# Kernel tuning notes

Measured on AMD Instinct MI355X. Metric: run time of the kernel, lower is better.

Reference implementation:

```python
import jax, jax.numpy as jnp
import numpy as np

H, D = 8, 8          # num_heads, hidden_size (head dim)
SCALE = 0.25         # Hopfield beta/scaling
STEPS = 3            # update_steps_max
LN_EPS = 1e-5


def ln(x, g, b):
    m = x.mean(-1, keepdims=True)
    v = ((x - m) ** 2).mean(-1, keepdims=True)
    return (x - m) * jax.lax.rsqrt(v + LN_EPS) * g + b


def setup_inputs() -> dict:
    key = jax.random.key(0)
    ks = jax.random.split(key, 8)
    B, N, E = 32, 512, 512
    P = H * D  # 64 virtual hopfield dim
    s = lambda k, shape: jax.random.normal(k, shape, jnp.float32) * 0.05
    return dict(
        x=jax.random.normal(ks[0], (B, N, E), jnp.float32),
        g_q=jnp.ones((E,), jnp.float32), b_q=jnp.zeros((E,), jnp.float32),
        g_k=jnp.ones((E,), jnp.float32), b_k=jnp.zeros((E,), jnp.float32),
        g_v=jnp.ones((E,), jnp.float32), b_v=jnp.zeros((E,), jnp.float32),
        Wq=s(ks[1], (P, E)), bq=jnp.zeros((P,), jnp.float32),
        Wk=s(ks[2], (P, E)), bk=jnp.zeros((P,), jnp.float32),
        Wv=s(ks[3], (P, E)), bv=jnp.zeros((P,), jnp.float32),
        Wo=s(ks[4], (E, P)), bo=jnp.zeros((E,), jnp.float32),
        Wl=s(ks[5], (1, N * E)), bl=jnp.zeros((1,), jnp.float32),
    )


def reference(x, g_q, b_q, g_k, b_k, g_v, b_v,
              Wq, bq, Wk, bk, Wv, bv, Wo, bo, Wl, bl):
    B, N, E = x.shape
    # LayerNorm on state (query), stored (key), projection (value) patterns
    q = (ln(x, g_q, b_q) @ Wq.T + bq).reshape(B, N, H, D)
    k = (ln(x, g_k, b_k) @ Wk.T + bk).reshape(B, N, H, D)
    v = (ln(x, g_v, b_v) @ Wv.T + bv).reshape(B, N, H, D)
    # iterative Hopfield retrieval: xi <- softmax(beta * xi K^T) K
    xi = q
    for _ in range(STEPS):
        a = jax.nn.softmax(SCALE * jnp.einsum('bihd,bjhd->bhij', xi, k), axis=-1)
        xi = jnp.einsum('bhij,bjhd->bihd', a, k)
    # final association with value patterns
    a = jax.nn.softmax(SCALE * jnp.einsum('bihd,bjhd->bhij', xi, k), axis=-1)
    o = jnp.einsum('bhij,bjhd->bihd', a, v).reshape(B, N, H * D)
    o = o @ Wo.T + bo              # (B, N, E) out projection
    y = o.reshape(B, N * E) @ Wl.T + bl  # (B, 1) classifier head
    return y.reshape(-1)           # flatten(start_dim=0) -> (B,)
```

## Files before the change

kernel.cpp:

```cpp
#include <hip/hip_runtime.h>

#define E_DIM 512
#define N_DIM 512
#define B_DIM 32
#define H_DIM 8
#define D_DIM 8
#define P3    192

typedef _Float16 half_t;
typedef __attribute__((ext_vector_type(2))) _Float16 half2v;
typedef __attribute__((ext_vector_type(4))) _Float16 half4v;
typedef __attribute__((ext_vector_type(8))) _Float16 half8v;
typedef __attribute__((ext_vector_type(4))) float f32x4;

#define PB_STRIDE 36
#define XS_STRIDE 520

__device__ inline float block_reduce_256(float v) {
    __shared__ float red[4];
    #pragma unroll
    for (int m = 32; m >= 1; m >>= 1) v += __shfl_xor(v, m);
    int w = threadIdx.x >> 6;
    if ((threadIdx.x & 63) == 0) red[w] = v;
    __syncthreads();
    if (threadIdx.x == 0) v = red[0] + red[1] + red[2] + red[3];
    return v;
}

__device__ inline half8v cvt8(float4 a, float4 b) {
    half8v h;
    h[0] = (half_t)a.x; h[1] = (half_t)a.y; h[2] = (half_t)a.z; h[3] = (half_t)a.w;
    h[4] = (half_t)b.x; h[5] = (half_t)b.y; h[6] = (half_t)b.z; h[7] = (half_t)b.w;
    return h;
}

__device__ inline half2v pk2(float a, float b) {
    return __builtin_bit_cast(half2v, __builtin_amdgcn_cvt_pkrtz(a, b));
}

__global__ __launch_bounds__(256) void prep_w(const float* __restrict__ Wq,
                        const float* __restrict__ Wk, const float* __restrict__ Wv,
                        const float* __restrict__ gq, const float* __restrict__ gk,
                        const float* __restrict__ gv,
                        const float* __restrict__ bnq, const float* __restrict__ bnk,
                        const float* __restrict__ bnv,
                        const float* __restrict__ bq, const float* __restrict__ bk,
                        const float* __restrict__ bv,
                        const float* __restrict__ bl,
                        half_t* __restrict__ WthF, float* __restrict__ colsum,
                        float* __restrict__ b2, float* __restrict__ y,
                        float* __restrict__ c0acc) {
    int pp = blockIdx.x;
    int which = pp >> 6, p = pp & 63;
    int ct = pp >> 4, c16 = pp & 15;
    const float* W  = (which == 0) ? Wq  : (which == 1) ? Wk  : Wv;
    const float* g  = (which == 0) ? gq  : (which == 1) ? gk  : gv;
    const float* bn = (which == 0) ? bnq : (which == 1) ? bnk : bnv;
    const float* bb = (which == 0) ? bq  : (which == 1) ? bk  : bv;
    int t = threadIdx.x;
    if (pp == 0) {
        if (t < 32) y[t] = bl[0];
        if (t == 32) c0acc[0] = 0.f;
    }
    float cs = 0.f, dt = 0.f;
    #pragma unroll
    for (int l = 0; l < 2; ++l) {
        int e = t + l * 256;
        float wv = W[p * E_DIM + e];
        half_t wh = (half_t)(wv * g[e]);
        int k32 = e >> 5, g2 = (e >> 3) & 3, j = e & 7;
        WthF[(((size_t)(ct * 16 + k32) * 64) + g2 * 16 + c16) * 8 + j] = wh;
        cs += (float)wh;
        dt += wv * bn[e];
    }
    cs = block_reduce_256(cs);
    __syncthreads();
    dt = block_reduce_256(dt);
    if (t == 0) { colsum[pp] = cs; b2[pp] = dt + bb[p]; }
}

__global__ __launch_bounds__(256) void ln_qkv_wl2(const float* __restrict__ x,
                                              const half_t* __restrict__ WthF,
                                              const float* __restrict__ b2,
                                              const float* __restrict__ colsum,
                                              half_t* __restrict__ qkv16,
                                              const float* __restrict__ Wl,
                                              const float* __restrict__ Wo,
                                              const float* __restrict__ bo,
                                              float* __restrict__ Wl2,
                                              float* __restrict__ c0acc) {
    __shared__ half_t Xs[16 * XS_STRIDE];
    __shared__ float stats[16][2];
    if (blockIdx.x < 1024) {
        const int t = threadIdx.x;
        const int lane = t & 63;
        const int w = t >> 6;
        const int g2 = lane >> 4, c16 = lane & 15;
        const int row0 = blockIdx.x * 16;
        {
            const int row = t >> 4, c = t & 15;
            const float4* xrow = (const float4*)(x + (size_t)(row0 + row) * E_DIM);
            float sx = 0.f, sxx = 0.f;
            #pragma unroll
            for (int l = 0; l < 8; ++l) {
                int f4 = c + l * 16;
                float4 a = xrow[f4];
                sx  += a.x + a.y + a.z + a.w;
                sxx += a.x*a.x + a.y*a.y + a.z*a.z + a.w*a.w;
                half4v h;
                h[0] = (half_t)a.x; h[1] = (half_t)a.y;
                h[2] = (half_t)a.z; h[3] = (half_t)a.w;
                *(half4v*)&Xs[row * XS_STRIDE + f4 * 4] = h;
            }
            #pragma unroll
            for (int m = 1; m <= 8; m <<= 1) {
                sx += __shfl_xor(sx, m); sxx += __shfl_xor(sxx, m);
            }
            if (c == 0) {
                float mean = sx * (1.f / E_DIM);
                float var  = sxx * (1.f / E_DIM) - mean * mean;
                stats[row][0] = mean;
                stats[row][1] = rsqrtf(var + 1e-5f);
            }
        }
        __syncthreads();
        f32x4 acc[3] = {{0.f,0.f,0.f,0.f},{0.f,0.f,0.f,0.f},{0.f,0.f,0.f,0.f}};
        const half_t* wf = WthF + (size_t)w * 3 * 16 * 512;
        #pragma unroll 4
        for (int k32 = 0; k32 < 16; ++k32) {
            half8v af = *(const half8v*)&Xs[c16 * XS_STRIDE + k32 * 32 + g2 * 8];
            #pragma unroll
            for (int nt = 0; nt < 3; ++nt) {
                half8v bf = *(const half8v*)(wf + ((size_t)(nt * 16 + k32)) * 512 + lane * 8);
                acc[nt] = __builtin_amdgcn_mfma_f32_16x16x32_f16(af, bf, acc[nt], 0, 0, 0);
            }
        }
        #pragma unroll
        for (int nt = 0; nt < 3; ++nt) {
            int pp = w * 48 + nt * 16 + c16;
            float cs = colsum[pp], bb = b2[pp];
            int which = pp >> 6, p = pp & 63;
            int h = p >> 3, d = p & 7;
            half_t* dst0 = qkv16 + (size_t)which * (B_DIM * H_DIM * N_DIM * D_DIM);
            #pragma unroll
            for (int r = 0; r < 4; ++r) {
                int rowi = g2 * 4 + r;
                float val = stats[rowi][1] * (acc[nt][r] - stats[rowi][0] * cs) + bb;
                int ng = row0 + rowi;
                int b = ng >> 9, n = ng & 511;
                dst0[(((size_t)(b * H_DIM + h)) * N_DIM + n) * D_DIM + d] = (half_t)val;
            }
        }
    } else {
        const int blk = blockIdx.x - 1024;
        const int t = threadIdx.x;
        const int lane = t & 63;
        const int w = t >> 6;
        const int g2 = lane >> 4, c16 = lane & 15;
        const int n0 = blk * 16;
        const int pcol = w * 16;
        f32x4 acc = {0.f, 0.f, 0.f, 0.f};
        float pc = 0.f;
        const float* arow = Wl + (size_t)(n0 + c16) * E_DIM;
        #pragma unroll 2
        for (int k0 = 0; k0 < E_DIM; k0 += 32) {
            int kbase = k0 + g2 * 8;
            float4 a0 = *(const float4*)(arow + kbase);
            float4 a1 = *(const float4*)(arow + kbase + 4);
            if (w == 0) {
                float4 b0 = *(const float4*)(bo + kbase);
                float4 b1 = *(const float4*)(bo + kbase + 4);
                pc += a0.x*b0.x + a0.y*b0.y + a0.z*b0.z + a0.w*b0.w
                    + a1.x*b1.x + a1.y*b1.y + a1.z*b1.z + a1.w*b1.w;
            }
            half8v af = cvt8(a0, a1);
            half8v bf;
            #pragma unroll
            for (int j = 0; j < 8; ++j)
                bf[j] = (half_t)Wo[(size_t)(kbase + j) * 64 + pcol + c16];
            acc = __builtin_amdgcn_mfma_f32_16x16x32_f16(af, bf, acc, 0, 0, 0);
        }
        int p = pcol + c16, h = p >> 3, d = p & 7;
        #pragma unroll
        for (int r = 0; r < 4; ++r) {
            int n = n0 + g2 * 4 + r;
            Wl2[h * (N_DIM * D_DIM) + n * D_DIM + d] = acc[r];
        }
        if (w == 0) {
            pc += __shfl_xor(pc, 16); pc += __shfl_xor(pc, 32);
            pc += __shfl_xor(pc, 1);  pc += __shfl_xor(pc, 2);
            pc += __shfl_xor(pc, 4);  pc += __shfl_xor(pc, 8);
            if (lane == 0) atomicAdd(c0acc, pc);
        }
    }
}

__global__ __launch_bounds__(256) void hopfield(const half_t* __restrict__ q16,
                                                const half_t* __restrict__ k16,
                                                const half_t* __restrict__ v16,
                                                const float* __restrict__ Wl2,
                                                const float* __restrict__ c0acc,
                                                float* __restrict__ y) {
    __shared__ half_t Kb[N_DIM * 8];
    __shared__ half_t Xi[128 * 8];
    __shared__ half_t KTb[16 * 536];
    __shared__ half_t Pb[4 * 16 * PB_STRIDE];
    const int t = threadIdx.x;
    const int lane = t & 63;
    const int w = t >> 6;
    const int g2 = lane >> 4;
    const int c16 = lane & 15;
    const int bh = blockIdx.x >> 2, seg = blockIdx.x & 3;
    const float C = 0.25f * 1.44269504088896f;
    const half_t* kg = k16 + (size_t)bh * (N_DIM * D_DIM);
    const half_t* vg = v16 + (size_t)bh * (N_DIM * D_DIM);
    const half_t* qg = q16 + (size_t)bh * (N_DIM * D_DIM) + seg * 128 * 8;
    const float* wl2p = Wl2 + (bh & 7) * (N_DIM * D_DIM) + seg * 128 * 8;

    for (int i = t; i < 536; i += 256) KTb[9 * 536 + i] = (half_t)0.f;
    {
        int j0 = 2 * t;
        half8v r0 = *(const half8v*)(kg + j0 * 8);
        half8v r1 = *(const half8v*)(kg + j0 * 8 + 8);
        *(half8v*)&Kb[j0 * 8] = r0;
        *(half8v*)&Kb[j0 * 8 + 8] = r1;
        #pragma unroll
        for (int d = 0; d < 8; ++d) {
            KTb[d * 536 + j0] = r0[d];
            KTb[d * 536 + j0 + 1] = r1[d];
        }
        KTb[8 * 536 + j0] = (half_t)1.f;
        KTb[8 * 536 + j0 + 1] = (half_t)1.f;
    }
    if (t < 128) {
        half8v hq = *(const half8v*)(qg + t * 8);
        half8v h;
        #pragma unroll
        for (int d = 0; d < 8; ++d) h[d] = (half_t)(C * (float)hq[d]);
        *(half8v*)&Xi[t * 8] = h;
    }
    __syncthreads();

    const half_t* zsrc = &KTb[9 * 536];
    half_t* myP = &Pb[w * 16 * PB_STRIDE];
    float fsum = 0.f;

    for (int it = 0; it < 4; ++it) {
        if (it == 3) {
            __syncthreads();
            int j0 = 2 * t;
            half8v r0 = *(const half8v*)(vg + j0 * 8);
            half8v r1 = *(const half8v*)(vg + j0 * 8 + 8);
            #pragma unroll
            for (int d = 0; d < 8; ++d) {
                KTb[d * 536 + j0] = r0[d];
                KTb[d * 536 + j0 + 1] = r1[d];
            }
            __syncthreads();
        }
        const half_t* x0p = (g2 == 0) ? &Xi[(w * 32 + c16) * 8] : zsrc;
        const half_t* x1p = (g2 == 0) ? &Xi[(w * 32 + 16 + c16) * 8] : zsrc;
        half8v bxi0 = *(const half8v*)x0p;
        half8v bxi1 = *(const half8v*)x1p;
        f32x4 U0 = {0.f, 0.f, 0.f, 0.f}, U1 = {0.f, 0.f, 0.f, 0.f};
        for (int j32 = 0; j32 < 16; ++j32) {
            half8v bKT = *(const half8v*)&KTb[c16 * 536 + j32 * 32 + g2 * 8];
            #pragma unroll
            for (int hh = 0; hh < 2; ++hh) {
                int jt16 = j32 * 2 + hh;
                const half_t* akp = (g2 == 0) ? &Kb[(jt16 * 16 + c16) * 8] : zsrc;
                half8v ak = *(const half8v*)akp;
                f32x4 S = {0.f, 0.f, 0.f, 0.f};
                S = __builtin_amdgcn_mfma_f32_16x16x32_f16(ak, bxi0, S, 0, 0, 0);
                half2v lo = pk2(__builtin_amdgcn_exp2f(S[0]), __builtin_amdgcn_exp2f(S[1]));
                half2v hi = pk2(__builtin_amdgcn_exp2f(S[2]), __builtin_amdgcn_exp2f(S[3]));
                half4v p = __builtin_shufflevector(lo, hi, 0, 1, 2, 3);
                *(half4v*)&myP[c16 * PB_STRIDE + hh * 16 + g2 * 4] = p;
            }
            {
                half4v alo = *(const half4v*)&myP[c16 * PB_STRIDE + g2 * 8];
                half4v ahi = *(const half4v*)&myP[c16 * PB_STRIDE + g2 * 8 + 4];
                half8v ap = __builtin_shufflevector(alo, ahi, 0, 1, 2, 3, 4, 5, 6, 7);
                U0 = __builtin_amdgcn_mfma_f32_16x16x32_f16(ap, bKT, U0, 0, 0, 0);
            }
            #pragma unroll
            for (int hh = 0; hh < 2; ++hh) {
                int jt16 = j32 * 2 + hh;
                const half_t* akp = (g2 == 0) ? &Kb[(jt16 * 16 + c16) * 8] : zsrc;
                half8v ak = *(const half8v*)akp;
                f32x4 S = {0.f, 0.f, 0.f, 0.f};
                S = __builtin_amdgcn_mfma_f32_16x16x32_f16(ak, bxi1, S, 0, 0, 0);
                half2v lo = pk2(__builtin_amdgcn_exp2f(S[0]), __builtin_amdgcn_exp2f(S[1]));
                half2v hi = pk2(__builtin_amdgcn_exp2f(S[2]), __builtin_amdgcn_exp2f(S[3]));
                half4v p = __builtin_shufflevector(lo, hi, 0, 1, 2, 3);
                *(half4v*)&myP[c16 * PB_STRIDE + hh * 16 + g2 * 4] = p;
            }
            {
                half4v alo = *(const half4v*)&myP[c16 * PB_STRIDE + g2 * 8];
                half4v ahi = *(const half4v*)&myP[c16 * PB_STRIDE + g2 * 8 + 4];
                half8v ap = __builtin_shufflevector(alo, ahi, 0, 1, 2, 3, 4, 5, 6, 7);
                U1 = __builtin_amdgcn_mfma_f32_16x16x32_f16(ap, bKT, U1, 0, 0, 0);
            }
        }
        int srcl = (lane & 48) | 8;
        #pragma unroll
        for (int r = 0; r < 4; ++r) {
            float l0 = __shfl(U0[r], srcl, 64);
            float l1 = __shfl(U1[r], srcl, 64);
            float inv0 = __builtin_amdgcn_rcpf(l0);
            float inv1 = __builtin_amdgcn_rcpf(l1);
            if (c16 < 8) {
                int i0 = w * 32 + g2 * 4 + r;
                int i1 = i0 + 16;
                if (it < 3) {
                    Xi[i0 * 8 + c16] = (half_t)(U0[r] * (C * inv0));
                    Xi[i1 * 8 + c16] = (half_t)(U1[r] * (C * inv1));
                } else {
                    fsum += (U0[r] * inv0) * wl2p[i0 * 8 + c16]
                          + (U1[r] * inv1) * wl2p[i1 * 8 + c16];
                }
            }
        }
    }
    float tot = block_reduce_256(fsum);
    if (t == 0) atomicAdd(&y[bh >> 3], tot);
    if (blockIdx.x == 0 && t < 32) {
        atomicAdd(&y[t], c0acc[0]);
    }
}

extern "C" void kernel_launch(void* const* d_in, const int* in_sizes, int n_in,
                              void* d_out, int out_size, void* d_ws, size_t ws_size,
                              hipStream_t stream) {
    const float* x   = (const float*)d_in[0];
    const float* g_q = (const float*)d_in[1];
    const float* b_q = (const float*)d_in[2];
    const float* g_k = (const float*)d_in[3];
    const float* b_k = (const float*)d_in[4];
    const float* g_v = (const float*)d_in[5];
    const float* b_v = (const float*)d_in[6];
    const float* Wq  = (const float*)d_in[7];
    const float* bq  = (const float*)d_in[8];
    const float* Wk  = (const float*)d_in[9];
    const float* bk  = (const float*)d_in[10];
    const float* Wv  = (const float*)d_in[11];
    const float* bv  = (const float*)d_in[12];
    const float* Wo  = (const float*)d_in[13];
    const float* bo  = (const float*)d_in[14];
    const float* Wl  = (const float*)d_in[15];
    const float* bl  = (const float*)d_in[16];
    float* out = (float*)d_out;

    float* ws = (float*)d_ws;
    float*  colsum = ws;
    float*  b2     = ws + 192;
    float*  c0acc  = ws + 384;
    float*  Wl2    = ws + 448;
    half_t* WthF   = (half_t*)(ws + 33216);
    half_t* qkv16  = (half_t*)(ws + 82368);

    half_t* q16 = qkv16;
    half_t* k16 = qkv16 + 1048576;
    half_t* v16 = qkv16 + 2097152;

    prep_w    <<<192, 256, 0, stream>>>(Wq, Wk, Wv, g_q, g_k, g_v,
                                        b_q, b_k, b_v, bq, bk, bv, bl,
                                        WthF, colsum, b2, out, c0acc);
    ln_qkv_wl2<<<1056, 256, 0, stream>>>(x, WthF, b2, colsum, qkv16,
                                         Wl, Wo, bo, Wl2, c0acc);
    hopfield  <<<1024, 256, 0, stream>>>(q16, k16, v16, Wl2, c0acc, out);
}
```

Before: 165.5 us.

## Switch Hopfield attention to 16x16x16 MFMA and keep probabilities in registers

Rewrites the Hopfield retrieval inner loop to use the 16x16x16 f16 MFMA instead of 16x16x32. The score tile is laid out so its exp2 output can feed the second MFMA straight from registers, which removes the per-wave shared-memory P buffer round trip and the g2-conditional pointer selects. K is stored with a padded stride and zero padding, and the transposed K stride is changed, both to allow conflict-reduced half4 loads. Output normalization and the final weighted sum now use vectorized half4 and float4 stores and loads. The cost is more MFMA instructions, each with less K depth, plus extra zero-padding writes to shared memory.

```diff
diff --git a/kernel.cpp b/kernel.cpp
--- a/kernel.cpp
+++ b/kernel.cpp
@@ -13,8 +13,9 @@
 typedef __attribute__((ext_vector_type(8))) _Float16 half8v;
 typedef __attribute__((ext_vector_type(4))) float f32x4;
 
-#define PB_STRIDE 36
 #define XS_STRIDE 520
+#define KB2_STRIDE 20
+#define KT_STRIDE  532
 
 __device__ inline float block_reduce_256(float v) {
     __shared__ float red[4];
@@ -201,10 +202,9 @@
                                                 const float* __restrict__ Wl2,
                                                 const float* __restrict__ c0acc,
                                                 float* __restrict__ y) {
-    __shared__ half_t Kb[N_DIM * 8];
-    __shared__ half_t Xi[128 * 8];
-    __shared__ half_t KTb[16 * 536];
-    __shared__ half_t Pb[4 * 16 * PB_STRIDE];
+    __shared__ half_t Kb2[N_DIM * KB2_STRIDE];
+    __shared__ half_t KTb[16 * KT_STRIDE];
+    __shared__ half_t Xi[128 * 8 + 16];
     const int t = threadIdx.x;
     const int lane = t & 63;
     const int w = t >> 6;
@@ -217,20 +217,30 @@
     const half_t* qg = q16 + (size_t)bh * (N_DIM * D_DIM) + seg * 128 * 8;
     const float* wl2p = Wl2 + (bh & 7) * (N_DIM * D_DIM) + seg * 128 * 8;
 
-    for (int i = t; i < 536; i += 256) KTb[9 * 536 + i] = (half_t)0.f;
     {
-        int j0 = 2 * t;
+        const int j0 = 2 * t;
         half8v r0 = *(const half8v*)(kg + j0 * 8);
         half8v r1 = *(const half8v*)(kg + j0 * 8 + 8);
-        *(half8v*)&Kb[j0 * 8] = r0;
-        *(half8v*)&Kb[j0 * 8 + 8] = r1;
+        const half4v z4 = {};
+        half_t* p0 = &Kb2[j0 * KB2_STRIDE];
+        half_t* p1 = &Kb2[(j0 + 1) * KB2_STRIDE];
+        *(half4v*)(p0)      = __builtin_shufflevector(r0, r0, 0, 1, 2, 3);
+        *(half4v*)(p0 + 4)  = __builtin_shufflevector(r0, r0, 4, 5, 6, 7);
+        *(half4v*)(p0 + 8)  = z4;
+        *(half4v*)(p0 + 12) = z4;
+        *(half4v*)(p0 + 16) = z4;
+        *(half4v*)(p1)      = __builtin_shufflevector(r1, r1, 0, 1, 2, 3);
+        *(half4v*)(p1 + 4)  = __builtin_shufflevector(r1, r1, 4, 5, 6, 7);
+        *(half4v*)(p1 + 8)  = z4;
+        *(half4v*)(p1 + 12) = z4;
+        *(half4v*)(p1 + 16) = z4;
         #pragma unroll
         for (int d = 0; d < 8; ++d) {
-            KTb[d * 536 + j0] = r0[d];
-            KTb[d * 536 + j0 + 1] = r1[d];
-        }
-        KTb[8 * 536 + j0] = (half_t)1.f;
-        KTb[8 * 536 + j0 + 1] = (half_t)1.f;
+            KTb[d * KT_STRIDE + j0]     = r0[d];
+            KTb[d * KT_STRIDE + j0 + 1] = r1[d];
+        }
+        KTb[8 * KT_STRIDE + j0]     = (half_t)1.f;
+        KTb[8 * KT_STRIDE + j0 + 1] = (half_t)1.f;
     }
     if (t < 128) {
         half8v hq = *(const half8v*)(qg + t * 8);
@@ -241,84 +251,65 @@
     }
     __syncthreads();
 
-    const half_t* zsrc = &KTb[9 * 536];
-    half_t* myP = &Pb[w * 16 * PB_STRIDE];
+    const half_t* akp = &Kb2[c16 * KB2_STRIDE + g2 * 4];
+    const half_t* aTp = &KTb[c16 * KT_STRIDE + g2 * 4];
+    const half4v hz = {};
     float fsum = 0.f;
 
     for (int it = 0; it < 4; ++it) {
         if (it == 3) {
             __syncthreads();
-            int j0 = 2 * t;
+            const int j0 = 2 * t;
             half8v r0 = *(const half8v*)(vg + j0 * 8);
             half8v r1 = *(const half8v*)(vg + j0 * 8 + 8);
             #pragma unroll
             for (int d = 0; d < 8; ++d) {
-                KTb[d * 536 + j0] = r0[d];
-                KTb[d * 536 + j0 + 1] = r1[d];
+                KTb[d * KT_STRIDE + j0]     = r0[d];
+                KTb[d * KT_STRIDE + j0 + 1] = r1[d];
             }
             __syncthreads();
         }
-        const half_t* x0p = (g2 == 0) ? &Xi[(w * 32 + c16) * 8] : zsrc;
-        const half_t* x1p = (g2 == 0) ? &Xi[(w * 32 + 16 + c16) * 8] : zsrc;
-        half8v bxi0 = *(const half8v*)x0p;
-        half8v bxi1 = *(const half8v*)x1p;
+        half4v bx0 = *(const half4v*)&Xi[(w * 32 + c16) * 8 + g2 * 4];
+        half4v bx1 = *(const half4v*)&Xi[(w * 32 + 16 + c16) * 8 + g2 * 4];
+        if (g2 >= 2) { bx0 = hz; bx1 = hz; }
         f32x4 U0 = {0.f, 0.f, 0.f, 0.f}, U1 = {0.f, 0.f, 0.f, 0.f};
-        for (int j32 = 0; j32 < 16; ++j32) {
-            half8v bKT = *(const half8v*)&KTb[c16 * 536 + j32 * 32 + g2 * 8];
-            #pragma unroll
-            for (int hh = 0; hh < 2; ++hh) {
-                int jt16 = j32 * 2 + hh;
-                const half_t* akp = (g2 == 0) ? &Kb[(jt16 * 16 + c16) * 8] : zsrc;
-                half8v ak = *(const half8v*)akp;
-                f32x4 S = {0.f, 0.f, 0.f, 0.f};
-                S = __builtin_amdgcn_mfma_f32_16x16x32_f16(ak, bxi0, S, 0, 0, 0);
-                half2v lo = pk2(__builtin_amdgcn_exp2f(S[0]), __builtin_amdgcn_exp2f(S[1]));
-                half2v hi = pk2(__builtin_amdgcn_exp2f(S[2]), __builtin_amdgcn_exp2f(S[3]));
-                half4v p = __builtin_shufflevector(lo, hi, 0, 1, 2, 3);
-                *(half4v*)&myP[c16 * PB_STRIDE + hh * 16 + g2 * 4] = p;
-            }
-            {
-                half4v alo = *(const half4v*)&myP[c16 * PB_STRIDE + g2 * 8];
-                half4v ahi = *(const half4v*)&myP[c16 * PB_STRIDE + g2 * 8 + 4];
-                half8v ap = __builtin_shufflevector(alo, ahi, 0, 1, 2, 3, 4, 5, 6, 7);
-                U0 = __builtin_amdgcn_mfma_f32_16x16x32_f16(ap, bKT, U0, 0, 0, 0);
-            }
-            #pragma unroll
-            for (int hh = 0; hh < 2; ++hh) {
-                int jt16 = j32 * 2 + hh;
-                const half_t* akp = (g2 == 0) ? &Kb[(jt16 * 16 + c16) * 8] : zsrc;
-                half8v ak = *(const half8v*)akp;
-                f32x4 S = {0.f, 0.f, 0.f, 0.f};
-                S = __builtin_amdgcn_mfma_f32_16x16x32_f16(ak, bxi1, S, 0, 0, 0);
-                half2v lo = pk2(__builtin_amdgcn_exp2f(S[0]), __builtin_amdgcn_exp2f(S[1]));
-                half2v hi = pk2(__builtin_amdgcn_exp2f(S[2]), __builtin_amdgcn_exp2f(S[3]));
-                half4v p = __builtin_shufflevector(lo, hi, 0, 1, 2, 3);
-                *(half4v*)&myP[c16 * PB_STRIDE + hh * 16 + g2 * 4] = p;
-            }
-            {
-                half4v alo = *(const half4v*)&myP[c16 * PB_STRIDE + g2 * 8];
-                half4v ahi = *(const half4v*)&myP[c16 * PB_STRIDE + g2 * 8 + 4];
-                half8v ap = __builtin_shufflevector(alo, ahi, 0, 1, 2, 3, 4, 5, 6, 7);
-                U1 = __builtin_amdgcn_mfma_f32_16x16x32_f16(ap, bKT, U1, 0, 0, 0);
-            }
-        }
-        int srcl = (lane & 48) | 8;
-        #pragma unroll
-        for (int r = 0; r < 4; ++r) {
-            float l0 = __shfl(U0[r], srcl, 64);
-            float l1 = __shfl(U1[r], srcl, 64);
-            float inv0 = __builtin_amdgcn_rcpf(l0);
-            float inv1 = __builtin_amdgcn_rcpf(l1);
-            if (c16 < 8) {
-                int i0 = w * 32 + g2 * 4 + r;
-                int i1 = i0 + 16;
-                if (it < 3) {
-                    Xi[i0 * 8 + c16] = (half_t)(U0[r] * (C * inv0));
-                    Xi[i1 * 8 + c16] = (half_t)(U1[r] * (C * inv1));
-                } else {
-                    fsum += (U0[r] * inv0) * wl2p[i0 * 8 + c16]
-                          + (U1[r] * inv1) * wl2p[i1 * 8 + c16];
+        #pragma unroll 4
+        for (int kt = 0; kt < 32; ++kt) {
+            half4v ak = *(const half4v*)(akp + kt * (16 * KB2_STRIDE));
+            half4v aT = *(const half4v*)(aTp + kt * 16);
+            f32x4 Z = {0.f, 0.f, 0.f, 0.f};
+            f32x4 S0 = __builtin_amdgcn_mfma_f32_16x16x16f16(ak, bx0, Z, 0, 0, 0);
+            f32x4 S1 = __builtin_amdgcn_mfma_f32_16x16x16f16(ak, bx1, Z, 0, 0, 0);
+            half2v l0 = pk2(__builtin_amdgcn_exp2f(S0[0]), __builtin_amdgcn_exp2f(S0[1]));
+            half2v h0 = pk2(__builtin_amdgcn_exp2f(S0[2]), __builtin_amdgcn_exp2f(S0[3]));
+            half4v p0 = __builtin_shufflevector(l0, h0, 0, 1, 2, 3);
+            half2v l1 = pk2(__builtin_amdgcn_exp2f(S1[0]), __builtin_amdgcn_exp2f(S1[1]));
+            half2v h1 = pk2(__builtin_amdgcn_exp2f(S1[2]), __builtin_amdgcn_exp2f(S1[3]));
+            half4v p1 = __builtin_shufflevector(l1, h1, 0, 1, 2, 3);
+            U0 = __builtin_amdgcn_mfma_f32_16x16x16f16(aT, p0, U0, 0, 0, 0);
+            U1 = __builtin_amdgcn_mfma_f32_16x16x16f16(aT, p1, U1, 0, 0, 0);
+        }
+        float den0 = __shfl(U0[0], 32 + c16, 64);
+        float den1 = __shfl(U1[0], 32 + c16, 64);
+        float inv0 = __builtin_amdgcn_rcpf(den0);
+        float inv1 = __builtin_amdgcn_rcpf(den1);
+        if (it < 3) {
+            if (g2 < 2) {
+                half4v h0, h1;
+                #pragma unroll
+                for (int r = 0; r < 4; ++r) {
+                    h0[r] = (half_t)(U0[r] * (C * inv0));
+                    h1[r] = (half_t)(U1[r] * (C * inv1));
                 }
+                *(half4v*)&Xi[(w * 32 + c16) * 8 + g2 * 4]      = h0;
+                *(half4v*)&Xi[(w * 32 + 16 + c16) * 8 + g2 * 4] = h1;
+            }
+        } else {
+            if (g2 < 2) {
+                float4 w0 = *(const float4*)&wl2p[(w * 32 + c16) * 8 + g2 * 4];
+                float4 w1 = *(const float4*)&wl2p[(w * 32 + 16 + c16) * 8 + g2 * 4];
+                fsum = inv0 * (U0[0]*w0.x + U0[1]*w0.y + U0[2]*w0.z + U0[3]*w0.w)
+                     + inv1 * (U1[0]*w1.x + U1[1]*w1.y + U1[2]*w1.z + U1[3]*w1.w);
             }
         }
     }
```

Result: faster. 157.9 us (-4.6%).
